# Kernel optimization log

Hardware: AMD Instinct MI355X
Metric: run time of the kernel (lower is better)

## Reference

```python
import jax, jax.numpy as jnp
import numpy as np

N = 50000
E = 1600000
IN_F = 512
OUT_F = 128
NEG_SLOPE = 0.01   # nn.LeakyReLU() default
TEMPERATURE = 0.5


def setup_inputs() -> dict:
    key = jax.random.key(0)
    k1, k2, k3, k4 = jax.random.split(key, 4)
    h = jax.random.normal(k1, (N, IN_F), dtype=jnp.float32)
    # xavier_uniform with gain=1.414
    limW = 1.414 * np.sqrt(6.0 / (IN_F + OUT_F))
    W = jax.random.uniform(k2, (IN_F, OUT_F), minval=-limW, maxval=limW, dtype=jnp.float32)
    lima = 1.414 * np.sqrt(6.0 / (2 * OUT_F + 1))
    a = jax.random.uniform(k3, (2 * OUT_F, 1), minval=-lima, maxval=lima, dtype=jnp.float32)
    edge_index = jax.random.randint(k4, (2, E), 0, N, dtype=jnp.int64)
    return {"h": h, "W": W, "a": a, "edge_index": edge_index}


def reference(h, W, a, edge_index):
    # Inference: F.dropout(training=False) is identity.
    Wh = h @ W                                   # [N, F_out]
    src = edge_index[0]                          # row indices -> softmax segments
    dst = edge_index[1]
    # cat([Wh[src], Wh[dst]]) @ a == (Wh @ a1)[src] + (Wh @ a2)[dst]
    a1 = a[:OUT_F, 0]
    a2 = a[OUT_F:, 0]
    s1 = Wh @ a1                                 # [N]
    s2 = Wh @ a2                                 # [N]
    e = s1[src] + s2[dst]                        # [E]
    e = jnp.where(e >= 0, e, NEG_SLOPE * e)      # LeakyReLU
    logits = e / TEMPERATURE
    # sparse softmax over dim=1 (per source-node row segments)
    seg_max = jax.ops.segment_max(logits, src, num_segments=N)  # [N]
    ex = jnp.exp(logits - seg_max[src])          # [E]
    denom = jax.ops.segment_sum(ex, src, num_segments=N)        # [N]
    att = ex / denom[src]                        # [E]
    # sparse-dense matmul: h_prime[i] = sum_j att(i,j) * Wh[j]
    h_prime = jax.ops.segment_sum(att[:, None] * Wh[dst], src, num_segments=N)  # [N, F_out]
    return jax.nn.relu(h_prime)                  # concat=True path
```

## Files before the change

kernel.cpp:

```cpp
#include <hip/hip_runtime.h>
#include <cstdint>
#include <cstddef>

#define N_NODES 50000
#define N_EDGES 1600000
#define IN_FEAT 512
#define OUT_FEAT 128
#define NEG_SLOPE 0.01f
#define INV_TEMP 2.0f
#define PAD_DEG 128

#define BUCKETS 400
#define BNODES 125
#define BCAP 5000
#define A_BLOCKS 250
#define A_EPC (N_EDGES / A_BLOCKS)
#define A_G4 (A_EPC / 4)

typedef __attribute__((ext_vector_type(8))) short short8;
typedef __attribute__((ext_vector_type(4))) float f32x4;

#define GLOBAL_AS __attribute__((address_space(1)))
#define LDS_AS __attribute__((address_space(3)))

__device__ inline unsigned short f2bf(float x) {
    unsigned int u = __float_as_uint(x);
    unsigned int r = (u + 0x7fffu + ((u >> 16) & 1u)) >> 16;
    return (unsigned short)r;
}
__device__ inline float bf2f(unsigned short b) {
    return __uint_as_float(((unsigned int)b) << 16);
}


__global__ __launch_bounds__(256) void binA_kernel(const int* __restrict__ src,
                                                   const int* __restrict__ dst,
                                                   int* __restrict__ bucket_cursor,
                                                   int* __restrict__ binned) {
    __shared__ int cntL[BUCKETS];
    __shared__ int baseL[BUCKETS];
    int t = threadIdx.x;
    for (int i = t; i < BUCKETS; i += 256) cntL[i] = 0;
    __syncthreads();
    size_t ebase = (size_t)blockIdx.x * A_EPC;

    for (int g = t; g < A_G4; g += 256) {
        int4 s4 = *(const int4*)(src + ebase + (size_t)g * 4);
#pragma unroll
        for (int j = 0; j < 4; ++j) {
            int s = (&s4.x)[j];
            atomicAdd(&cntL[s / BNODES], 1);
        }
    }
    __syncthreads();
    for (int i = t; i < BUCKETS; i += 256) {
        int c = cntL[i];
        baseL[i] = c ? atomicAdd(&bucket_cursor[i], c) : 0;
        cntL[i] = 0;
    }
    __syncthreads();
    for (int g = t; g < A_G4; g += 256) {
        int4 s4 = *(const int4*)(src + ebase + (size_t)g * 4);
        int4 d4 = *(const int4*)(dst + ebase + (size_t)g * 4);
#pragma unroll
        for (int j = 0; j < 4; ++j) {
            int s = (&s4.x)[j];
            int b = s / BNODES;
            int sl = s - b * BNODES;
            int pos = atomicAdd(&cntL[b], 1);
            int slot = baseL[b] + pos;
            if (slot < BCAP)
                binned[(size_t)b * BCAP + slot] = (sl << 16) | (&d4.x)[j];
        }
    }
}


__global__ __launch_bounds__(256) void binB_kernel(const int* __restrict__ bucket_cursor,
                                                   const int* __restrict__ binned,
                                                   int* __restrict__ cnt,
                                                   int* __restrict__ csr) {
    __shared__ int cL[BNODES];
    int b = blockIdx.x;
    int t = threadIdx.x;
    if (t < BNODES) cL[t] = 0;
    __syncthreads();
    int m = min(bucket_cursor[b], BCAP);
    const int* bp = binned + (size_t)b * BCAP;
    int n0 = b * BNODES;
    for (int i = t; i < m; i += 256) {
        int p = bp[i];
        int sl = p >> 16;
        int d = p & 0xFFFF;
        int pos = atomicAdd(&cL[sl], 1);
        if (pos < PAD_DEG) csr[(size_t)(n0 + sl) * PAD_DEG + pos] = d;
    }
    __syncthreads();
    if (t < BNODES) cnt[n0 + t] = min(cL[t], PAD_DEG);
}

__global__ __launch_bounds__(256) void convert_w_kernel(const float* __restrict__ W,
                                                        unsigned short* __restrict__ Wt,
                                                        int* __restrict__ bucket_cursor) {
    int tid = blockIdx.x * blockDim.x + threadIdx.x;
    if (tid < BUCKETS) bucket_cursor[tid] = 0;
    if (tid >= IN_FEAT * OUT_FEAT) return;
    int n = tid >> 9;
    int k = tid & 511;
    Wt[tid] = f2bf(W[k * OUT_FEAT + n]);
}


__global__ __launch_bounds__(256) void mfma_gemm_kernel(const float* __restrict__ h,
                                                        const unsigned short* __restrict__ Wt,
                                                        const float* __restrict__ a_vec,
                                                        unsigned short* __restrict__ Whb,
                                                        float* __restrict__ s1,
                                                        float* __restrict__ s2) {
    __shared__ unsigned short lA[4 * 2 * 64 * 8];
    __shared__ unsigned short lB[8 * 2 * 64 * 8];

    int t = threadIdx.x;
    int w = t >> 6;
    int L = t & 63;
    int m0 = blockIdx.x * 64;

    int arow = m0 + w * 16 + (L & 15);
    bool arow_ok = arow < N_NODES;
    int kq = (L >> 4) * 8;

    f32x4 acc[8];
#pragma unroll
    for (int i = 0; i < 8; ++i) acc[i] = (f32x4){0.f, 0.f, 0.f, 0.f};

    for (int k0 = 0; k0 < IN_FEAT; k0 += 64) {
        float4 av[2][2];
#pragma unroll
        for (int c = 0; c < 2; ++c) {
            av[c][0] = make_float4(0.f, 0.f, 0.f, 0.f);
            av[c][1] = make_float4(0.f, 0.f, 0.f, 0.f);
        }
        if (arow_ok) {
            const float* arp = h + (size_t)arow * IN_FEAT + k0 + kq;
            av[0][0] = *(const float4*)(arp);
            av[0][1] = *(const float4*)(arp + 4);
            av[1][0] = *(const float4*)(arp + 32);
            av[1][1] = *(const float4*)(arp + 36);
        }
#pragma unroll
        for (int c = 0; c < 4; ++c) {
            int nb = w * 2 + (c >> 1);
            int ksub = c & 1;
            const GLOBAL_AS unsigned short* g =
                (const GLOBAL_AS unsigned short*)(Wt + (size_t)(nb * 16 + (L & 15)) * IN_FEAT +
                                                  (k0 + ksub * 32 + kq));
            LDS_AS unsigned short* lp = (LDS_AS unsigned short*)(lB + (nb * 2 + ksub) * 512);
            __builtin_amdgcn_global_load_lds((const GLOBAL_AS void*)g, (LDS_AS void*)lp, 16, 0, 0);
        }
#pragma unroll
        for (int c = 0; c < 2; ++c) {
            short8 v;
            v[0] = (short)f2bf(av[c][0].x); v[1] = (short)f2bf(av[c][0].y);
            v[2] = (short)f2bf(av[c][0].z); v[3] = (short)f2bf(av[c][0].w);
            v[4] = (short)f2bf(av[c][1].x); v[5] = (short)f2bf(av[c][1].y);
            v[6] = (short)f2bf(av[c][1].z); v[7] = (short)f2bf(av[c][1].w);
            *(short8*)(lA + ((w * 2 + c) * 64 + L) * 8) = v;
        }
        __syncthreads();
#pragma unroll
        for (int ksub = 0; ksub < 2; ++ksub) {
            short8 af = *(const short8*)(lA + ((w * 2 + ksub) * 64 + L) * 8);
#pragma unroll
            for (int nb = 0; nb < 8; ++nb) {
                short8 bf = *(const short8*)(lB + ((nb * 2 + ksub) * 64 + L) * 8);
                acc[nb] = __builtin_amdgcn_mfma_f32_16x16x32_bf16(af, bf, acc[nb], 0, 0, 0);
            }
        }
        __syncthreads();
    }

    int col0 = L & 15;
    int rbase = m0 + w * 16 + (L >> 4) * 4;

    float a1c[8], a2c[8];
#pragma unroll
    for (int nb = 0; nb < 8; ++nb) {
        a1c[nb] = a_vec[nb * 16 + col0];
        a2c[nb] = a_vec[128 + nb * 16 + col0];
    }

#pragma unroll
    for (int r = 0; r < 4; ++r) {
        int row = rbase + r;
        bool ok = row < N_NODES;
        float p1 = 0.f, p2 = 0.f;
        if (ok) {
            unsigned short* orow = Whb + (size_t)row * OUT_FEAT;
#pragma unroll
            for (int nb = 0; nb < 8; ++nb) {
                float v = acc[nb][r];
                orow[nb * 16 + col0] = f2bf(v);
                p1 = fmaf(v, a1c[nb], p1);
                p2 = fmaf(v, a2c[nb], p2);
            }
        }
#pragma unroll
        for (int off = 8; off > 0; off >>= 1) {
            p1 += __shfl_xor(p1, off, 64);
            p2 += __shfl_xor(p2, off, 64);
        }
        if (ok && col0 == 0) {
            s1[row] = p1;
            s2[row] = p2;
        }
    }
}


__global__ __launch_bounds__(256) void node_kernel(const unsigned short* __restrict__ Whb,
                                                   const float* __restrict__ s1,
                                                   const float* __restrict__ s2,
                                                   const int* __restrict__ cnt,
                                                   const int* __restrict__ csr,
                                                   float* __restrict__ out) {
    int lane = threadIdx.x & 63;
    int w = threadIdx.x >> 6;
    int n = blockIdx.x * 4 + w;
    if (n >= N_NODES) return;
    int deg = cnt[n];
    size_t start = (size_t)n * PAD_DEG;
    int g = lane >> 4;
    int fo = lane & 15;

    float accv[8];
#pragma unroll
    for (int f = 0; f < 8; ++f) accv[f] = 0.f;
    float inv = 0.f;

    if (deg > 0) {
        float s1n = s1[n];
        int d0 = 0, d1 = 0;
        float ex0 = 0.f, ex1 = 0.f;
        if (lane < deg) {
            d0 = csr[start + lane];
            float ev = s1n + s2[d0];
            ev = ev >= 0.f ? ev : NEG_SLOPE * ev;
            ex0 = __expf(ev * INV_TEMP);
        }
        if (lane + 64 < deg) {
            d1 = csr[start + lane + 64];
            float ev = s1n + s2[d1];
            ev = ev >= 0.f ? ev : NEG_SLOPE * ev;
            ex1 = __expf(ev * INV_TEMP);
        }
        float denom = ex0 + ex1;
#pragma unroll
        for (int off = 32; off > 0; off >>= 1) denom += __shfl_xor(denom, off, 64);
        inv = 1.0f / denom;

#pragma unroll 2
        for (int jj = 0; jj < deg; jj += 4) {
            int e = jj + g;
            bool hi = jj >= 64;
            float exs = hi ? ex1 : ex0;
            int dsel = hi ? d1 : d0;
            float p = __shfl(exs, e & 63, 64);
            int dd = __shfl(dsel, e & 63, 64);
            short8 row = *(const short8*)(Whb + (size_t)dd * OUT_FEAT + fo * 8);
#pragma unroll
            for (int f = 0; f < 8; ++f)
                accv[f] = fmaf(p, bf2f((unsigned short)row[f]), accv[f]);
        }
#pragma unroll
        for (int f = 0; f < 8; ++f) {
            accv[f] += __shfl_xor(accv[f], 16, 64);
            accv[f] += __shfl_xor(accv[f], 32, 64);
        }
    }

    if (g == 0) {
        float* orow = out + (size_t)n * OUT_FEAT + fo * 8;
        float4 o0, o1;
        o0.x = fmaxf(accv[0] * inv, 0.f); o0.y = fmaxf(accv[1] * inv, 0.f);
        o0.z = fmaxf(accv[2] * inv, 0.f); o0.w = fmaxf(accv[3] * inv, 0.f);
        o1.x = fmaxf(accv[4] * inv, 0.f); o1.y = fmaxf(accv[5] * inv, 0.f);
        o1.z = fmaxf(accv[6] * inv, 0.f); o1.w = fmaxf(accv[7] * inv, 0.f);
        *(float4*)(orow) = o0;
        *(float4*)(orow + 4) = o1;
    }
}


extern "C" void kernel_launch(void* const* d_in, const int* in_sizes, int n_in,
                              void* d_out, int out_size, void* d_ws, size_t ws_size,
                              hipStream_t stream) {
    const float* h = (const float*)d_in[0];
    const float* W = (const float*)d_in[1];
    const float* a = (const float*)d_in[2];
    const int* edge = (const int*)d_in[3];
    const int* src = edge;
    const int* dst = edge + N_EDGES;
    float* out = (float*)d_out;

    char* ws = (char*)d_ws;
    size_t off = 0;
    auto alloc = [&](size_t bytes) -> void* {
        void* p = ws + off;
        off = (off + bytes + 255) & ~(size_t)255;
        return p;
    };
    unsigned short* Whb = (unsigned short*)alloc((size_t)N_NODES * OUT_FEAT * sizeof(unsigned short));
    float* s1 = (float*)alloc((size_t)N_NODES * sizeof(float));
    float* s2 = (float*)alloc((size_t)N_NODES * sizeof(float));
    int* cnt = (int*)alloc((size_t)N_NODES * sizeof(int));
    int* csr = (int*)alloc((size_t)N_NODES * PAD_DEG * sizeof(int));
    unsigned short* Wt = (unsigned short*)alloc((size_t)IN_FEAT * OUT_FEAT * sizeof(unsigned short));
    int* bucket_cursor = (int*)alloc((size_t)BUCKETS * sizeof(int));
    int* binned = (int*)alloc((size_t)BUCKETS * BCAP * sizeof(int));

    convert_w_kernel<<<(IN_FEAT * OUT_FEAT + 255) / 256, 256, 0, stream>>>(W, Wt, bucket_cursor);
    binA_kernel<<<A_BLOCKS, 256, 0, stream>>>(src, dst, bucket_cursor, binned);
    binB_kernel<<<BUCKETS, 256, 0, stream>>>(bucket_cursor, binned, cnt, csr);
    mfma_gemm_kernel<<<(N_NODES + 63) / 64, 256, 0, stream>>>(h, Wt, a, Whb, s1, s2);
    node_kernel<<<(N_NODES + 3) / 4, 256, 0, stream>>>(Whb, s1, s2, cnt, csr, out);
}
```

Baseline: 269.9 us.

## Restructure GEMM to LDS-free register tiling and retune binning kernels

```diff
diff --git a/kernel.cpp b/kernel.cpp
--- a/kernel.cpp
+++ b/kernel.cpp
@@ -13,15 +13,12 @@
 #define BUCKETS 400
 #define BNODES 125
 #define BCAP 5000
-#define A_BLOCKS 250
+#define A_BLOCKS 500
 #define A_EPC (N_EDGES / A_BLOCKS)
 #define A_G4 (A_EPC / 4)
 
 typedef __attribute__((ext_vector_type(8))) short short8;
 typedef __attribute__((ext_vector_type(4))) float f32x4;
-
-#define GLOBAL_AS __attribute__((address_space(1)))
-#define LDS_AS __attribute__((address_space(3)))
 
 __device__ inline unsigned short f2bf(float x) {
     unsigned int u = __float_as_uint(x);
@@ -53,10 +50,13 @@
         }
     }
     __syncthreads();
+    int rot = blockIdx.x % BUCKETS;
     for (int i = t; i < BUCKETS; i += 256) {
-        int c = cntL[i];
-        baseL[i] = c ? atomicAdd(&bucket_cursor[i], c) : 0;
-        cntL[i] = 0;
+        int ii = i + rot;
+        if (ii >= BUCKETS) ii -= BUCKETS;
+        int c = cntL[ii];
+        baseL[ii] = c ? atomicAdd(&bucket_cursor[ii], c) : 0;
+        cntL[ii] = 0;
     }
     __syncthreads();
     for (int g = t; g < A_G4; g += 256) {
@@ -76,7 +76,7 @@
 }
 
 
-__global__ __launch_bounds__(256) void binB_kernel(const int* __restrict__ bucket_cursor,
+__global__ __launch_bounds__(512) void binB_kernel(const int* __restrict__ bucket_cursor,
                                                    const int* __restrict__ binned,
                                                    int* __restrict__ cnt,
                                                    int* __restrict__ csr) {
@@ -88,7 +88,7 @@
     int m = min(bucket_cursor[b], BCAP);
     const int* bp = binned + (size_t)b * BCAP;
     int n0 = b * BNODES;
-    for (int i = t; i < m; i += 256) {
+    for (int i = t; i < m; i += 512) {
         int p = bp[i];
         int sl = p >> 16;
         int d = p & 0xFFFF;
@@ -117,71 +117,49 @@
                                                         unsigned short* __restrict__ Whb,
                                                         float* __restrict__ s1,
                                                         float* __restrict__ s2) {
-    __shared__ unsigned short lA[4 * 2 * 64 * 8];
-    __shared__ unsigned short lB[8 * 2 * 64 * 8];
-
     int t = threadIdx.x;
     int w = t >> 6;
     int L = t & 63;
-    int m0 = blockIdx.x * 64;
-
-    int arow = m0 + w * 16 + (L & 15);
-    bool arow_ok = arow < N_NODES;
+    int m0 = blockIdx.x * 128 + w * 32;
     int kq = (L >> 4) * 8;
 
-    f32x4 acc[8];
-#pragma unroll
-    for (int i = 0; i < 8; ++i) acc[i] = (f32x4){0.f, 0.f, 0.f, 0.f};
-
-    for (int k0 = 0; k0 < IN_FEAT; k0 += 64) {
-        float4 av[2][2];
-#pragma unroll
-        for (int c = 0; c < 2; ++c) {
-            av[c][0] = make_float4(0.f, 0.f, 0.f, 0.f);
-            av[c][1] = make_float4(0.f, 0.f, 0.f, 0.f);
-        }
-        if (arow_ok) {
-            const float* arp = h + (size_t)arow * IN_FEAT + k0 + kq;
-            av[0][0] = *(const float4*)(arp);
-            av[0][1] = *(const float4*)(arp + 4);
-            av[1][0] = *(const float4*)(arp + 32);
-            av[1][1] = *(const float4*)(arp + 36);
-        }
-#pragma unroll
-        for (int c = 0; c < 4; ++c) {
-            int nb = w * 2 + (c >> 1);
-            int ksub = c & 1;
-            const GLOBAL_AS unsigned short* g =
-                (const GLOBAL_AS unsigned short*)(Wt + (size_t)(nb * 16 + (L & 15)) * IN_FEAT +
-                                                  (k0 + ksub * 32 + kq));
-            LDS_AS unsigned short* lp = (LDS_AS unsigned short*)(lB + (nb * 2 + ksub) * 512);
-            __builtin_amdgcn_global_load_lds((const GLOBAL_AS void*)g, (LDS_AS void*)lp, 16, 0, 0);
-        }
-#pragma unroll
-        for (int c = 0; c < 2; ++c) {
-            short8 v;
-            v[0] = (short)f2bf(av[c][0].x); v[1] = (short)f2bf(av[c][0].y);
-            v[2] = (short)f2bf(av[c][0].z); v[3] = (short)f2bf(av[c][0].w);
-            v[4] = (short)f2bf(av[c][1].x); v[5] = (short)f2bf(av[c][1].y);
-            v[6] = (short)f2bf(av[c][1].z); v[7] = (short)f2bf(av[c][1].w);
-            *(short8*)(lA + ((w * 2 + c) * 64 + L) * 8) = v;
-        }
-        __syncthreads();
-#pragma unroll
-        for (int ksub = 0; ksub < 2; ++ksub) {
-            short8 af = *(const short8*)(lA + ((w * 2 + ksub) * 64 + L) * 8);
-#pragma unroll
-            for (int nb = 0; nb < 8; ++nb) {
-                short8 bf = *(const short8*)(lB + ((nb * 2 + ksub) * 64 + L) * 8);
-                acc[nb] = __builtin_amdgcn_mfma_f32_16x16x32_bf16(af, bf, acc[nb], 0, 0, 0);
-            }
-        }
-        __syncthreads();
+    int r0 = m0 + (L & 15);
+    int r1 = r0 + 16;
+    bool ok0 = r0 < N_NODES, ok1 = r1 < N_NODES;
+    const float* h0 = h + (size_t)(ok0 ? r0 : 0) * IN_FEAT + kq;
+    const float* h1 = h + (size_t)(ok1 ? r1 : 0) * IN_FEAT + kq;
+    const unsigned short* bb = Wt + (size_t)(L & 15) * IN_FEAT + kq;
+
+    f32x4 acc[2][8];
+#pragma unroll
+    for (int mi = 0; mi < 2; ++mi)
+#pragma unroll
+        for (int nb = 0; nb < 8; ++nb) acc[mi][nb] = (f32x4){0.f, 0.f, 0.f, 0.f};
+
+#pragma unroll 2
+    for (int k0 = 0; k0 < IN_FEAT; k0 += 32) {
+        float4 a0lo = *(const float4*)(h0 + k0);
+        float4 a0hi = *(const float4*)(h0 + k0 + 4);
+        float4 a1lo = *(const float4*)(h1 + k0);
+        float4 a1hi = *(const float4*)(h1 + k0 + 4);
+        short8 af0, af1;
+        af0[0] = (short)f2bf(a0lo.x); af0[1] = (short)f2bf(a0lo.y);
+        af0[2] = (short)f2bf(a0lo.z); af0[3] = (short)f2bf(a0lo.w);
+        af0[4] = (short)f2bf(a0hi.x); af0[5] = (short)f2bf(a0hi.y);
+        af0[6] = (short)f2bf(a0hi.z); af0[7] = (short)f2bf(a0hi.w);
+        af1[0] = (short)f2bf(a1lo.x); af1[1] = (short)f2bf(a1lo.y);
+        af1[2] = (short)f2bf(a1lo.z); af1[3] = (short)f2bf(a1lo.w);
+        af1[4] = (short)f2bf(a1hi.x); af1[5] = (short)f2bf(a1hi.y);
+        af1[6] = (short)f2bf(a1hi.z); af1[7] = (short)f2bf(a1hi.w);
+#pragma unroll
+        for (int nb = 0; nb < 8; ++nb) {
+            short8 bf = *(const short8*)(bb + (size_t)nb * 16 * IN_FEAT + k0);
+            acc[0][nb] = __builtin_amdgcn_mfma_f32_16x16x32_bf16(af0, bf, acc[0][nb], 0, 0, 0);
+            acc[1][nb] = __builtin_amdgcn_mfma_f32_16x16x32_bf16(af1, bf, acc[1][nb], 0, 0, 0);
+        }
     }
 
     int col0 = L & 15;
-    int rbase = m0 + w * 16 + (L >> 4) * 4;
-
     float a1c[8], a2c[8];
 #pragma unroll
     for (int nb = 0; nb < 8; ++nb) {
@@ -190,28 +168,32 @@
     }
 
 #pragma unroll
-    for (int r = 0; r < 4; ++r) {
-        int row = rbase + r;
-        bool ok = row < N_NODES;
-        float p1 = 0.f, p2 = 0.f;
-        if (ok) {
-            unsigned short* orow = Whb + (size_t)row * OUT_FEAT;
-#pragma unroll
-            for (int nb = 0; nb < 8; ++nb) {
-                float v = acc[nb][r];
-                orow[nb * 16 + col0] = f2bf(v);
-                p1 = fmaf(v, a1c[nb], p1);
-                p2 = fmaf(v, a2c[nb], p2);
+    for (int mi = 0; mi < 2; ++mi) {
+        int rbase = m0 + mi * 16 + (L >> 4) * 4;
+#pragma unroll
+        for (int r = 0; r < 4; ++r) {
+            int row = rbase + r;
+            bool ok = row < N_NODES;
+            float p1 = 0.f, p2 = 0.f;
+            if (ok) {
+                unsigned short* orow = Whb + (size_t)row * OUT_FEAT;
+#pragma unroll
+                for (int nb = 0; nb < 8; ++nb) {
+                    float v = acc[mi][nb][r];
+                    orow[nb * 16 + col0] = f2bf(v);
+                    p1 = fmaf(v, a1c[nb], p1);
+                    p2 = fmaf(v, a2c[nb], p2);
+                }
             }
-        }
-#pragma unroll
-        for (int off = 8; off > 0; off >>= 1) {
-            p1 += __shfl_xor(p1, off, 64);
-            p2 += __shfl_xor(p2, off, 64);
-        }
-        if (ok && col0 == 0) {
-            s1[row] = p1;
-            s2[row] = p2;
+#pragma unroll
+            for (int off = 8; off > 0; off >>= 1) {
+                p1 += __shfl_xor(p1, off, 64);
+                p2 += __shfl_xor(p2, off, 64);
+            }
+            if (ok && col0 == 0) {
+                s1[row] = p1;
+                s2[row] = p2;
+            }
         }
     }
 }
@@ -320,7 +302,7 @@
 
     convert_w_kernel<<<(IN_FEAT * OUT_FEAT + 255) / 256, 256, 0, stream>>>(W, Wt, bucket_cursor);
     binA_kernel<<<A_BLOCKS, 256, 0, stream>>>(src, dst, bucket_cursor, binned);
-    binB_kernel<<<BUCKETS, 256, 0, stream>>>(bucket_cursor, binned, cnt, csr);
-    mfma_gemm_kernel<<<(N_NODES + 63) / 64, 256, 0, stream>>>(h, Wt, a, Whb, s1, s2);
+    binB_kernel<<<BUCKETS, 512, 0, stream>>>(bucket_cursor, binned, cnt, csr);
+    mfma_gemm_kernel<<<(N_NODES + 127) / 128, 256, 0, stream>>>(h, Wt, a, Whb, s1, s2);
     node_kernel<<<(N_NODES + 3) / 4, 256, 0, stream>>>(Whb, s1, s2, cnt, csr, out);
 }
```

After: 286.3 us. 1.06x slower.
